# Kernel tuning notes

Measured on AMD Instinct MI355X. Metric: run time of the kernel, lower is better.

Reference implementation:

```python
import jax, jax.numpy as jnp
import numpy as np

BN_EPS = 1e-5


def setup_inputs() -> dict:
    key = jax.random.key(0)
    ks = jax.random.split(key, 8)
    B, N, D = 16, 16384, 64
    NP, NS = 1024, 32
    inp = {
        "xyz": jax.random.normal(ks[0], (B, 3, N), dtype=jnp.float32),
        "points": jax.random.normal(ks[1], (B, D, N), dtype=jnp.float32),
        "fps_init": jax.random.randint(ks[2], (B,), 0, N, dtype=jnp.int32),
        "group_idx": jax.random.randint(ks[3], (B, NP, NS), 0, N, dtype=jnp.int32),
    }
    chans = [67, 64, 128, 128]
    for i in range(3):
        cin, cout = chans[i], chans[i + 1]
        wk = jax.random.fold_in(ks[4], i)
        inp[f"W{i}"] = jax.random.normal(wk, (cout, cin), dtype=jnp.float32) * (1.0 / np.sqrt(cin))
        inp[f"b{i}"] = jnp.zeros((cout,), dtype=jnp.float32)
        inp[f"g{i}"] = jnp.ones((cout,), dtype=jnp.float32)
        inp[f"be{i}"] = jnp.zeros((cout,), dtype=jnp.float32)
    return inp


def _fps(x, init_far, npoint):
    # x: [B,N,3]; iterative furthest point sampling, npoint sequential steps
    B, N, _ = x.shape

    def step(carry, _):
        dist, far = carry
        c = jnp.take_along_axis(x, far[:, None, None], axis=1)  # [B,1,3]
        d = jnp.sum((x - c) ** 2, axis=-1)                       # [B,N]
        dist = jnp.minimum(dist, d)
        return (dist, jnp.argmax(dist, axis=-1).astype(far.dtype)), far

    init = (jnp.full((B, N), 1e10, dtype=x.dtype), init_far)
    _, cents = jax.lax.scan(step, init, None, length=npoint)
    return cents.T  # [B, npoint]


def _conv_bn_relu(h, W, b, g, be):
    # h: [B, np, ns, Cin]; 1x1 conv == channel matmul; BN (training stats) over (B,np,ns)
    y = jnp.einsum('bskc,oc->bsko', h, W) + b
    m = y.mean(axis=(0, 1, 2))
    v = y.var(axis=(0, 1, 2))
    y = (y - m) * jax.lax.rsqrt(v + BN_EPS) * g + be
    return jax.nn.relu(y)


def reference(xyz, points, fps_init, group_idx,
              W0, b0, g0, be0, W1, b1, g1, be1, W2, b2, g2, be2):
    x = jnp.transpose(xyz, (0, 2, 1))     # [B,N,3]
    p = jnp.transpose(points, (0, 2, 1))  # [B,N,D]
    B, N, _ = x.shape
    NP, NS = group_idx.shape[1], group_idx.shape[2]

    cents = _fps(x, fps_init, NP)                                   # [B,NP]
    new_xyz = jnp.take_along_axis(x, cents[:, :, None], axis=1)     # [B,NP,3]

    flat = group_idx.reshape(B, NP * NS)
    gx = jnp.take_along_axis(x, flat[:, :, None], axis=1).reshape(B, NP, NS, 3)
    gp = jnp.take_along_axis(p, flat[:, :, None], axis=1).reshape(B, NP, NS, -1)
    h = jnp.concatenate([gx, gp], axis=-1)  # [B,NP,NS,67]

    h = _conv_bn_relu(h, W0, b0, g0, be0)
    h = _conv_bn_relu(h, W1, b1, g1, be1)
    h = _conv_bn_relu(h, W2, b2, g2, be2)
    new_points = h.max(axis=2)              # max over nsample -> [B,NP,Cout]

    return jnp.transpose(new_xyz, (0, 2, 1)), jnp.transpose(new_points, (0, 2, 1))
```

## Files before the change

kernel.cpp:

```cpp
#include <hip/hip_runtime.h>

typedef short bf16x8 __attribute__((ext_vector_type(8)));
typedef float f32x4 __attribute__((ext_vector_type(4)));
typedef float f32x2 __attribute__((ext_vector_type(2)));
typedef unsigned short u16;
typedef unsigned int u32;
typedef unsigned long long u64;

#define NPTS 16384
#define NPOINT 1024
#define STOT 524288

__device__ __forceinline__ u16 f2bf(float f){
  u32 u = __builtin_bit_cast(u32, f);
  u += 0x7fffu + ((u >> 16) & 1u);
  return (u16)(u >> 16);
}
__device__ __forceinline__ float bf2f(u16 u){
  u32 x = ((u32)u) << 16;
  return __builtin_bit_cast(float, x);
}

template<int CTRL>
__device__ __forceinline__ u64 dpp_max(u64 key){
  u32 lo = (u32)key, hi = (u32)(key >> 32);
  u32 lo1 = (u32)__builtin_amdgcn_update_dpp(0, (int)lo, CTRL, 0xf, 0xf, true);
  u32 hi1 = (u32)__builtin_amdgcn_update_dpp(0, (int)hi, CTRL, 0xf, 0xf, true);
  u64 k1 = ((u64)hi1 << 32) | (u64)lo1;
  return (k1 > key) ? k1 : key;
}

__global__ __launch_bounds__(1024) void fps_kernel(const float* __restrict__ xyz,
                                                   const int* __restrict__ finit,
                                                   float4* __restrict__ xpk_all,
                                                   float* __restrict__ out0){
  __shared__ u64 warr[2][16];
  const int b = blockIdx.x, t = threadIdx.x;
  const int wave = t >> 6, lane = t & 63;
  const float* xb = xyz + (size_t)b * 3 * NPTS;
  float4* xpk = xpk_all + (size_t)b * NPTS;
  f32x2 px[8], py[8], pz[8], dist[8];
#pragma unroll
  for (int j = 0; j < 8; j++){
    f32x2 x, y, z;
#pragma unroll
    for (int h = 0; h < 2; h++){
      int n = ((2*j + h) << 10) + t;
      x[h] = xb[n];
      y[h] = xb[NPTS + n];
      z[h] = xb[2*NPTS + n];
      xpk[n] = make_float4(x[h], y[h], z[h], 0.f);
    }
    px[j] = x; py[j] = y; pz[j] = z;
    f32x2 big = {1e10f, 1e10f};
    dist[j] = big;
  }
  if (t < 32) ((u64*)warr)[t] = 0ULL;
  const int far0 = finit[b];
  __syncthreads();
  int nbu = far0;
  for (int it = 0; it < NPOINT; it++){
    float4 cc = xpk[nbu];
    if (t == 0){
      out0[((size_t)b*3 + 0)*NPOINT + it] = cc.x;
      out0[((size_t)b*3 + 1)*NPOINT + it] = cc.y;
      out0[((size_t)b*3 + 2)*NPOINT + it] = cc.z;
    }
    float bv = -1.f; int bk = 0;
    {
#pragma clang fp contract(off)
      f32x2 cx2 = {cc.x, cc.x}, cy2 = {cc.y, cc.y}, cz2 = {cc.z, cc.z};
#pragma unroll
      for (int j = 0; j < 8; j++){
        f32x2 dx = px[j] - cx2;
        f32x2 dy = py[j] - cy2;
        f32x2 dz = pz[j] - cz2;
        f32x2 dd = dx*dx + dy*dy + dz*dz;
        f32x2 dm = __builtin_elementwise_min(dist[j], dd);
        dist[j] = dm;
        bool g0 = dm.x > bv;
        bv = g0 ? dm.x : bv;  bk = g0 ? (2*j)   : bk;
        bool g1 = dm.y > bv;
        bv = g1 ? dm.y : bv;  bk = g1 ? (2*j+1) : bk;
      }
    }
    int bi = (bk << 10) + t;
    u64 key = ((u64)__builtin_bit_cast(u32, bv) << 32) | (u64)(u32)(~(u32)bi);
    key = dpp_max<0xB1>(key);
    key = dpp_max<0x4E>(key);
    key = dpp_max<0x141>(key);
    key = dpp_max<0x140>(key);
    key = dpp_max<0x142>(key);
    key = dpp_max<0x143>(key);
    if (lane == 63) warr[it & 1][wave] = key;
    __syncthreads();
    u64 kv = warr[it & 1][lane & 15];
    kv = dpp_max<0xB1>(kv);
    kv = dpp_max<0x4E>(kv);
    kv = dpp_max<0x141>(kv);
    kv = dpp_max<0x140>(kv);
    int nb = (int)(~(u32)kv);
    nbu = __builtin_amdgcn_readfirstlane(nb);
  }
}

__global__ __launch_bounds__(256) void pack_kernel(const float* __restrict__ xyz,
                                                   const float* __restrict__ points,
                                                   u16* __restrict__ XP){
  __shared__ float ldsb[67*256];
  const int blk = blockIdx.x, t = threadIdx.x;
  const int b = blk >> 6;
  const int n0 = (blk & 63) << 8;
  for (int c = 0; c < 67; c++){
    const float* src = (c < 3) ? (xyz + ((size_t)b*3 + c)*NPTS)
                               : (points + ((size_t)b*64 + (c-3))*NPTS);
    ldsb[c*256 + t] = src[n0 + t];
  }
  __syncthreads();
  u16* dst = XP + ((size_t)b*NPTS + n0)*96;
  for (int itc = 0; itc < 12; itc++){
    int q = t + (itc << 8);
    int r = q / 12, ch = q % 12;
    u16 tmp[8];
#pragma unroll
    for (int j = 0; j < 8; j++){
      int c = ch*8 + j;
      tmp[j] = (c < 67) ? f2bf(ldsb[c*256 + r]) : (u16)0;
    }
    uint4 v;
    v.x = (u32)tmp[0] | ((u32)tmp[1] << 16);
    v.y = (u32)tmp[2] | ((u32)tmp[3] << 16);
    v.z = (u32)tmp[4] | ((u32)tmp[5] << 16);
    v.w = (u32)tmp[6] | ((u32)tmp[7] << 16);
    *(uint4*)(dst + q*8) = v;
  }
}

__global__ __launch_bounds__(256) void prep_small(const float* __restrict__ W0,
                                                  const float* __restrict__ W1,
                                                  const float* __restrict__ W2,
                                                  u16* __restrict__ W0bf,
                                                  u16* __restrict__ W1bf,
                                                  u16* __restrict__ W2bf,
                                                  float* __restrict__ statsF){
  const int blk = blockIdx.x, t = threadIdx.x;
  if (blk < 48){
#pragma unroll
    for (int k = 0; k < 4; k++) statsF[blk*1024 + k*256 + t] = 0.f;
  } else if (blk == 48){
    for (int i = t; i < 64*96; i += 256){
      int n = i / 96, k = i % 96;
      W0bf[i] = (k < 67) ? f2bf(W0[n*67 + k]) : (u16)0;
    }
  } else if (blk <= 50){
    for (int i = (blk-49)*256 + t; i < 128*64; i += 512) W1bf[i] = f2bf(W1[i]);
  } else if (blk <= 54){
    for (int i = (blk-51)*256 + t; i < 128*128; i += 1024) W2bf[i] = f2bf(W2[i]);
  }
}

__global__ __launch_bounds__(256) void l0_kernel(const u16* __restrict__ XP,
                                                 const int* __restrict__ gidx,
                                                 const u16* __restrict__ W0bf,
                                                 u16* __restrict__ y0,
                                                 float* __restrict__ bsum, float* __restrict__ bsqr){
  __shared__ float lsum[64], lsqr[64];
  const int blk = blockIdx.x, t = threadIdx.x;
  const int b = blk >> 8, j = blk & 255;
  const int wave = t >> 6, lane = t & 63, lrow = lane & 15, lq = lane >> 4;
  if (t < 64){ lsum[t] = 0.f; lsqr[t] = 0.f; }
  __syncthreads();
  const size_t srow = (size_t)blk * 128;
  const int m0 = wave*32 + lrow, m1 = m0 + 16;
  const int gbase = b*32768 + j*128;
  const int p0 = gidx[gbase + m0];
  const int p1 = gidx[gbase + m1];
  const bf16x8* ar0 = (const bf16x8*)(XP + ((size_t)b*NPTS + p0)*96);
  const bf16x8* ar1 = (const bf16x8*)(XP + ((size_t)b*NPTS + p1)*96);
  f32x4 acc[2][4];
#pragma unroll
  for (int mt = 0; mt < 2; mt++)
#pragma unroll
    for (int nt = 0; nt < 4; nt++){ f32x4 z = {0.f,0.f,0.f,0.f}; acc[mt][nt] = z; }
#pragma unroll
  for (int ks = 0; ks < 3; ks++){
    bf16x8 af0 = ar0[ks*4 + lq];
    bf16x8 af1 = ar1[ks*4 + lq];
#pragma unroll
    for (int nt = 0; nt < 4; nt++){
      bf16x8 bb = *(const bf16x8*)(W0bf + (nt*16 + lrow)*96 + ks*32 + lq*8);
      acc[0][nt] = __builtin_amdgcn_mfma_f32_16x16x32_bf16(af0, bb, acc[0][nt], 0, 0, 0);
      acc[1][nt] = __builtin_amdgcn_mfma_f32_16x16x32_bf16(af1, bb, acc[1][nt], 0, 0, 0);
    }
  }
#pragma unroll
  for (int nt = 0; nt < 4; nt++){
    float s = 0.f, s2 = 0.f;
#pragma unroll
    for (int mt = 0; mt < 2; mt++){
#pragma unroll
      for (int i = 0; i < 4; i++){
        float u = acc[mt][nt][i];
        s += u; s2 = fmaf(u, u, s2);
        int m = wave*32 + mt*16 + lq*4 + i;
        y0[(srow + m)*64 + nt*16 + lrow] = f2bf(u);
      }
    }
    s  += __shfl_xor(s, 16, 64);  s  += __shfl_xor(s, 32, 64);
    s2 += __shfl_xor(s2, 16, 64); s2 += __shfl_xor(s2, 32, 64);
    if (lane < 16){ atomicAdd(&lsum[nt*16 + lane], s); atomicAdd(&lsqr[nt*16 + lane], s2); }
  }
  __syncthreads();
  if (t < 64){
    int bkt = blk & 63;
    atomicAdd(&bsum[bkt*128 + t], lsum[t]);
    atomicAdd(&bsqr[bkt*128 + t], lsqr[t]);
  }
}

__global__ __launch_bounds__(128) void stats_kernel(const float* __restrict__ bsum,
                                                    const float* __restrict__ bsqr,
                                                    const float* __restrict__ g,
                                                    const float* __restrict__ be,
                                                    float* __restrict__ a, float* __restrict__ d, int C){
  const int c = threadIdx.x;
  if (c >= C) return;
  float s = 0.f, s2 = 0.f;
  for (int k = 0; k < 64; k++){ s += bsum[k*128 + c]; s2 += bsqr[k*128 + c]; }
  const float inv = 1.f / (float)STOT;
  float m = s * inv;
  float v = s2 * inv - m*m;
  float aa = g[c] / sqrtf(v + 1e-5f);
  a[c] = aa;
  d[c] = be[c] - m*aa;
}

__device__ __forceinline__ bf16x8 load_bn_relu(const u16* __restrict__ row, int ko,
                                               const float* __restrict__ av,
                                               const float* __restrict__ dv){
  uint4 r = *(const uint4*)(row + ko);
  u32 w[4] = {r.x, r.y, r.z, r.w};
  bf16x8 out;
#pragma unroll
  for (int jj = 0; jj < 8; jj++){
    u16 us = (u16)(w[jj >> 1] >> ((jj & 1) * 16));
    float h = fmaxf(fmaf(av[ko + jj], bf2f(us), dv[ko + jj]), 0.f);
    out[jj] = (short)f2bf(h);
  }
  return out;
}

__global__ __launch_bounds__(256) void l1_kernel(const u16* __restrict__ y0,
                                                 const u16* __restrict__ W1bf,
                                                 const float* __restrict__ a0, const float* __restrict__ d0,
                                                 u16* __restrict__ y1,
                                                 float* __restrict__ bsum, float* __restrict__ bsqr){
  __shared__ float lsum[128], lsqr[128];
  __shared__ float av[64], dv[64];
  const int blk = blockIdx.x, t = threadIdx.x;
  const int wave = t >> 6, lane = t & 63, lrow = lane & 15, lq = lane >> 4;
  if (t < 128){ lsum[t] = 0.f; lsqr[t] = 0.f; }
  if (t < 64){ av[t] = a0[t]; dv[t] = d0[t]; }
  __syncthreads();
  const size_t srow = (size_t)blk * 128;
  const int m0 = wave*32 + lrow, m1 = m0 + 16;
  const u16* row0 = y0 + (srow + m0)*64;
  const u16* row1 = y0 + (srow + m1)*64;
  f32x4 acc[2][8];
#pragma unroll
  for (int mt = 0; mt < 2; mt++)
#pragma unroll
    for (int nt = 0; nt < 8; nt++){ f32x4 z = {0.f,0.f,0.f,0.f}; acc[mt][nt] = z; }
#pragma unroll
  for (int ks = 0; ks < 2; ks++){
    const int ko = ks*32 + lq*8;
    bf16x8 af0 = load_bn_relu(row0, ko, av, dv);
    bf16x8 af1 = load_bn_relu(row1, ko, av, dv);
#pragma unroll
    for (int nt = 0; nt < 8; nt++){
      bf16x8 bb = *(const bf16x8*)(W1bf + (nt*16 + lrow)*64 + ko);
      acc[0][nt] = __builtin_amdgcn_mfma_f32_16x16x32_bf16(af0, bb, acc[0][nt], 0, 0, 0);
      acc[1][nt] = __builtin_amdgcn_mfma_f32_16x16x32_bf16(af1, bb, acc[1][nt], 0, 0, 0);
    }
  }
#pragma unroll
  for (int nt = 0; nt < 8; nt++){
    float s = 0.f, s2 = 0.f;
#pragma unroll
    for (int mt = 0; mt < 2; mt++){
#pragma unroll
      for (int i = 0; i < 4; i++){
        float u = acc[mt][nt][i];
        s += u; s2 = fmaf(u, u, s2);
        int m = wave*32 + mt*16 + lq*4 + i;
        y1[(srow + m)*128 + nt*16 + lrow] = f2bf(u);
      }
    }
    s  += __shfl_xor(s, 16, 64);  s  += __shfl_xor(s, 32, 64);
    s2 += __shfl_xor(s2, 16, 64); s2 += __shfl_xor(s2, 32, 64);
    if (lane < 16){ atomicAdd(&lsum[nt*16 + lane], s); atomicAdd(&lsqr[nt*16 + lane], s2); }
  }
  __syncthreads();
  if (t < 128){
    int bkt = blk & 63;
    atomicAdd(&bsum[bkt*128 + t], lsum[t]);
    atomicAdd(&bsqr[bkt*128 + t], lsqr[t]);
  }
}

__global__ __launch_bounds__(256) void l2_kernel(const u16* __restrict__ y1,
                                                 const u16* __restrict__ W2bf,
                                                 const float* __restrict__ a1, const float* __restrict__ d1,
                                                 float* __restrict__ maxb, float* __restrict__ minb,
                                                 float* __restrict__ bsum, float* __restrict__ bsqr){
  __shared__ float lsum[128], lsqr[128];
  __shared__ float av[128], dv[128];
  const int blk = blockIdx.x, t = threadIdx.x;
  const int wave = t >> 6, lane = t & 63, lrow = lane & 15, lq = lane >> 4;
  if (t < 128){ lsum[t] = 0.f; lsqr[t] = 0.f; av[t] = a1[t]; dv[t] = d1[t]; }
  __syncthreads();
  const size_t srow = (size_t)blk * 128;
  const int m0 = wave*32 + lrow, m1 = m0 + 16;
  const u16* row0 = y1 + (srow + m0)*128;
  const u16* row1 = y1 + (srow + m1)*128;
  f32x4 acc[2][8];
#pragma unroll
  for (int mt = 0; mt < 2; mt++)
#pragma unroll
    for (int nt = 0; nt < 8; nt++){ f32x4 z = {0.f,0.f,0.f,0.f}; acc[mt][nt] = z; }
#pragma unroll
  for (int ks = 0; ks < 4; ks++){
    const int ko = ks*32 + lq*8;
    bf16x8 af0 = load_bn_relu(row0, ko, av, dv);
    bf16x8 af1 = load_bn_relu(row1, ko, av, dv);
#pragma unroll
    for (int nt = 0; nt < 8; nt++){
      bf16x8 bb = *(const bf16x8*)(W2bf + (nt*16 + lrow)*128 + ko);
      acc[0][nt] = __builtin_amdgcn_mfma_f32_16x16x32_bf16(af0, bb, acc[0][nt], 0, 0, 0);
      acc[1][nt] = __builtin_amdgcn_mfma_f32_16x16x32_bf16(af1, bb, acc[1][nt], 0, 0, 0);
    }
  }
#pragma unroll
  for (int nt = 0; nt < 8; nt++){
    float s = 0.f, s2 = 0.f, mx = -3.4e38f, mn = 3.4e38f;
#pragma unroll
    for (int mt = 0; mt < 2; mt++){
#pragma unroll
      for (int i = 0; i < 4; i++){
        float u = acc[mt][nt][i];
        s += u; s2 = fmaf(u, u, s2);
        mx = fmaxf(mx, u); mn = fminf(mn, u);
      }
    }
    s  += __shfl_xor(s, 16, 64);  s  += __shfl_xor(s, 32, 64);
    s2 += __shfl_xor(s2, 16, 64); s2 += __shfl_xor(s2, 32, 64);
    mx = fmaxf(mx, __shfl_xor(mx, 16, 64)); mx = fmaxf(mx, __shfl_xor(mx, 32, 64));
    mn = fminf(mn, __shfl_xor(mn, 16, 64)); mn = fminf(mn, __shfl_xor(mn, 32, 64));
    if (lane < 16){
      size_t gi = ((size_t)blk*4 + wave)*128 + nt*16 + lane;
      maxb[gi] = mx; minb[gi] = mn;
      atomicAdd(&lsum[nt*16 + lane], s); atomicAdd(&lsqr[nt*16 + lane], s2);
    }
  }
  __syncthreads();
  if (t < 128){
    int bkt = blk & 63;
    atomicAdd(&bsum[bkt*128 + t], lsum[t]);
    atomicAdd(&bsqr[bkt*128 + t], lsqr[t]);
  }
}

__global__ __launch_bounds__(256) void final_kernel(const float* __restrict__ maxb,
                                                    const float* __restrict__ minb,
                                                    const float* __restrict__ a2, const float* __restrict__ d2,
                                                    float* __restrict__ out1){
  __shared__ float ldsb[64*129];
  __shared__ float av[128], dv[128];
  const int blk = blockIdx.x, t = threadIdx.x;
  const int b = blk >> 4, np0 = (blk & 15) << 6;
  if (t < 128){ av[t] = a2[t]; dv[t] = d2[t]; }
  __syncthreads();
  const size_t base = ((size_t)b*NPOINT + np0)*128;
  for (int itc = 0; itc < 32; itc++){
    int e = t + (itc << 8);
    int npl = e >> 7, c = e & 127;
    float a = av[c];
    float mxv = maxb[base + e], mnv = minb[base + e];
    float vsel = (a >= 0.f) ? mxv : mnv;
    ldsb[npl*129 + c] = fmaxf(fmaf(a, vsel, dv[c]), 0.f);
  }
  __syncthreads();
  for (int itc = 0; itc < 32; itc++){
    int e = t + (itc << 8);
    int c = e >> 6, npl = e & 63;
    out1[((size_t)b*128 + c)*NPOINT + np0 + npl] = ldsb[npl*129 + c];
  }
}

extern "C" void kernel_launch(void* const* d_in, const int* in_sizes, int n_in,
                              void* d_out, int out_size, void* d_ws, size_t ws_size,
                              hipStream_t stream) {
  const float* xyz    = (const float*)d_in[0];
  const float* points = (const float*)d_in[1];
  const int*   finit  = (const int*)d_in[2];
  const int*   gidx   = (const int*)d_in[3];
  const float* W0  = (const float*)d_in[4];
  const float* g0v = (const float*)d_in[6];
  const float* be0 = (const float*)d_in[7];
  const float* W1  = (const float*)d_in[8];
  const float* g1v = (const float*)d_in[10];
  const float* be1 = (const float*)d_in[11];
  const float* W2  = (const float*)d_in[12];
  const float* g2v = (const float*)d_in[14];
  const float* be2 = (const float*)d_in[15];

  float* out0 = (float*)d_out;
  float* out1 = out0 + 16*3*NPOINT;

  char* ws = (char*)d_ws;
  u16* XP = (u16*)ws;
  u16* y1 = (u16*)ws;
  u16* y0 = (u16*)(ws + 134217728);
  float4* xpk = (float4*)(ws + 134217728);
  float* maxb = (float*)(ws + 134217728);
  float* minb = (float*)(ws + 134217728 + 8388608);
  float* statsF = (float*)(ws + 201326592);
  float* bsum0 = statsF;          float* bsqr0 = statsF + 8192;
  float* bsum1 = statsF + 16384;  float* bsqr1 = statsF + 24576;
  float* bsum2 = statsF + 32768;  float* bsqr2 = statsF + 40960;
  float* a0 = statsF + 49152;       float* d0 = a0 + 128;
  float* a1 = statsF + 49152 + 256; float* d1 = a1 + 128;
  float* a2 = statsF + 49152 + 512; float* d2 = a2 + 128;
  u16* W0bf = (u16*)(statsF + 49920);
  u16* W1bf = W0bf + 64*96;
  u16* W2bf = W1bf + 128*64;

  fps_kernel<<<16, 1024, 0, stream>>>(xyz, finit, xpk, out0);
  prep_small<<<64, 256, 0, stream>>>(W0, W1, W2, W0bf, W1bf, W2bf, statsF);
  pack_kernel<<<1024, 256, 0, stream>>>(xyz, points, XP);
  l0_kernel<<<4096, 256, 0, stream>>>(XP, gidx, W0bf, y0, bsum0, bsqr0);
  stats_kernel<<<1, 128, 0, stream>>>(bsum0, bsqr0, g0v, be0, a0, d0, 64);
  l1_kernel<<<4096, 256, 0, stream>>>(y0, W1bf, a0, d0, y1, bsum1, bsqr1);
  stats_kernel<<<1, 128, 0, stream>>>(bsum1, bsqr1, g1v, be1, a1, d1, 128);
  l2_kernel<<<4096, 256, 0, stream>>>(y1, W2bf, a1, d1, maxb, minb, bsum2, bsqr2);
  stats_kernel<<<1, 128, 0, stream>>>(bsum2, bsqr2, g2v, be2, a2, d2, 128);
  final_kernel<<<256, 256, 0, stream>>>(maxb, minb, a2, d2, out1);
}
```

Measured before the change: 2.231 ms.

## Spatially sort FPS points into Morton buckets and skip far clusters

The FPS kernel now bins points into a 16^3 Morton grid, counting-sorts them so each wave owns spatially coherent clusters of 256 points, and computes a bounding sphere per cluster. Each iteration skips a cluster's distance update when the new centroid is provably too far to lower any distance below the cluster's current max, which cuts the per-iteration distance arithmetic. It adds a setup pass with LDS atomics and a prefix scan, more cross-wave partial keys, and relies on conservative bound margins to keep argmax results exact.

```diff
diff --git a/kernel.cpp b/kernel.cpp
--- a/kernel.cpp
+++ b/kernel.cpp
@@ -29,36 +29,127 @@
   u64 k1 = ((u64)hi1 << 32) | (u64)lo1;
   return (k1 > key) ? k1 : key;
 }
+__device__ __forceinline__ u64 umax64(u64 a, u64 b){ return (a > b) ? a : b; }
+__device__ __forceinline__ u64 packkey(float d, int idx){
+  return ((u64)__builtin_bit_cast(u32, d) << 32) | (u64)(u32)(~(u32)idx);
+}
+__device__ __forceinline__ u32 spread3(int v){
+  u32 x = (u32)v;
+  return (x & 1u) | ((x & 2u) << 2) | ((x & 4u) << 4) | ((x & 8u) << 6);
+}
+__device__ __forceinline__ float wred_sum(float v){
+#pragma unroll
+  for (int off = 1; off < 64; off <<= 1) v += __shfl_xor(v, off, 64);
+  return v;
+}
+__device__ __forceinline__ float wred_max(float v){
+#pragma unroll
+  for (int off = 1; off < 64; off <<= 1) v = fmaxf(v, __shfl_xor(v, off, 64));
+  return v;
+}
 
 __global__ __launch_bounds__(1024) void fps_kernel(const float* __restrict__ xyz,
                                                    const int* __restrict__ finit,
                                                    float4* __restrict__ xpk_all,
+                                                   float4* __restrict__ xps_all,
                                                    float* __restrict__ out0){
-  __shared__ u64 warr[2][16];
+  __shared__ u32 hist[4096];
+  __shared__ u32 wsum[16];
+  __shared__ u64 par[2][64];
   const int b = blockIdx.x, t = threadIdx.x;
   const int wave = t >> 6, lane = t & 63;
   const float* xb = xyz + (size_t)b * 3 * NPTS;
   float4* xpk = xpk_all + (size_t)b * NPTS;
+  float4* xps = xps_all + (size_t)b * NPTS;
+
+  for (int i = t; i < 4096; i += 1024) hist[i] = 0;
+  __syncthreads();
+  u32 cr[16];
+#pragma unroll
+  for (int k = 0; k < 16; k++){
+    int n = (k << 10) + t;
+    float x = xb[n], y = xb[NPTS + n], z = xb[2*NPTS + n];
+    xpk[n] = make_float4(x, y, z, 0.f);
+    int xi = (int)fminf(fmaxf((x + 4.5f)*1.7777778f, 0.f), 15.f);
+    int yi = (int)fminf(fmaxf((y + 4.5f)*1.7777778f, 0.f), 15.f);
+    int zi = (int)fminf(fmaxf((z + 4.5f)*1.7777778f, 0.f), 15.f);
+    u32 cell = spread3(xi) | (spread3(yi) << 1) | (spread3(zi) << 2);
+    u32 rank = atomicAdd(&hist[cell], 1u);
+    cr[k] = (cell << 16) | rank;
+  }
+  __syncthreads();
+  uint4 hv = *(const uint4*)&hist[4*t];
+  u32 s = hv.x + hv.y + hv.z + hv.w;
+  u32 sInc = s;
+#pragma unroll
+  for (int off = 1; off < 64; off <<= 1){
+    u32 nv = (u32)__shfl_up((int)sInc, off, 64);
+    if (lane >= off) sInc += nv;
+  }
+  if (lane == 63) wsum[wave] = sInc;
+  __syncthreads();
+  u32 wb = 0;
+#pragma unroll
+  for (int i = 0; i < 16; i++) if (i < wave) wb += wsum[i];
+  u32 ex = wb + sInc - s;
+  hist[4*t]   = ex;
+  hist[4*t+1] = ex + hv.x;
+  hist[4*t+2] = ex + hv.x + hv.y;
+  hist[4*t+3] = ex + hv.x + hv.y + hv.z;
+  __syncthreads();
+#pragma unroll
+  for (int k = 0; k < 16; k++){
+    int n = (k << 10) + t;
+    float4 pnt = xpk[n];
+    u32 cell = cr[k] >> 16, rank = cr[k] & 0xFFFFu;
+    u32 pos = hist[cell] + rank;
+    pnt.w = __int_as_float(n);
+    xps[pos] = pnt;
+  }
+  __syncthreads();
   f32x2 px[8], py[8], pz[8], dist[8];
-#pragma unroll
-  for (int j = 0; j < 8; j++){
-    f32x2 x, y, z;
-#pragma unroll
-    for (int h = 0; h < 2; h++){
-      int n = ((2*j + h) << 10) + t;
-      x[h] = xb[n];
-      y[h] = xb[NPTS + n];
-      z[h] = xb[2*NPTS + n];
-      xpk[n] = make_float4(x[h], y[h], z[h], 0.f);
-    }
-    px[j] = x; py[j] = y; pz[j] = z;
-    f32x2 big = {1e10f, 1e10f};
-    dist[j] = big;
-  }
-  if (t < 32) ((u64*)warr)[t] = 0ULL;
-  const int far0 = finit[b];
-  __syncthreads();
-  int nbu = far0;
+  int idxv[16];
+#pragma unroll
+  for (int q = 0; q < 4; q++){
+#pragma unroll
+    for (int jj = 0; jj < 4; jj++){
+      int pos = (wave << 10) + (q << 8) + (jj << 6) + lane;
+      float4 sp = xps[pos];
+      int pr = 2*q + (jj >> 1), hf = jj & 1;
+      px[pr][hf] = sp.x; py[pr][hf] = sp.y; pz[pr][hf] = sp.z;
+      dist[pr][hf] = 1e10f;
+      idxv[4*q + jj] = __float_as_int(sp.w);
+    }
+  }
+  float ctrx[4], ctry[4], ctrz[4], rad[4], bmax[4];
+  u64 kb[4];
+#pragma unroll
+  for (int q = 0; q < 4; q++){
+    f32x2 sx2 = px[2*q] + px[2*q+1];
+    f32x2 sy2 = py[2*q] + py[2*q+1];
+    f32x2 sz2 = pz[2*q] + pz[2*q+1];
+    float cx = wred_sum(sx2.x + sx2.y) * (1.f/256.f);
+    float cy = wred_sum(sy2.x + sy2.y) * (1.f/256.f);
+    float cz = wred_sum(sz2.x + sz2.y) * (1.f/256.f);
+    float m2 = 0.f;
+#pragma unroll
+    for (int pr = 0; pr < 2; pr++){
+#pragma unroll
+      for (int hf = 0; hf < 2; hf++){
+        float dx = px[2*q+pr][hf] - cx, dy = py[2*q+pr][hf] - cy, dz = pz[2*q+pr][hf] - cz;
+        m2 = fmaxf(m2, dx*dx + dy*dy + dz*dz);
+      }
+    }
+    m2 = wred_max(m2);
+    ctrx[q] = __builtin_bit_cast(float, __builtin_amdgcn_readfirstlane(__builtin_bit_cast(int, cx)));
+    ctry[q] = __builtin_bit_cast(float, __builtin_amdgcn_readfirstlane(__builtin_bit_cast(int, cy)));
+    ctrz[q] = __builtin_bit_cast(float, __builtin_amdgcn_readfirstlane(__builtin_bit_cast(int, cz)));
+    rad[q]  = sqrtf(m2) * 1.0001f + 1e-6f;
+    bmax[q] = 1e10f;
+    kb[q]   = 0ULL;
+  }
+  int nbu = finit[b];
+  int p = 0;
   for (int it = 0; it < NPOINT; it++){
     float4 cc = xpk[nbu];
     if (t == 0){
@@ -66,41 +157,55 @@
       out0[((size_t)b*3 + 1)*NPOINT + it] = cc.y;
       out0[((size_t)b*3 + 2)*NPOINT + it] = cc.z;
     }
-    float bv = -1.f; int bk = 0;
-    {
+#pragma unroll
+    for (int q = 0; q < 4; q++){
+      float exx = cc.x - ctrx[q], eyy = cc.y - ctry[q], ezz = cc.z - ctrz[q];
+      float sd = sqrtf(exx*exx + eyy*eyy + ezz*ezz);
+      float tt = sd * 0.999f - rad[q];
+      bool doit = !((tt > 0.f) && (tt*tt >= bmax[q]));
+      if (__builtin_amdgcn_readfirstlane((int)doit)){
+        {
 #pragma clang fp contract(off)
-      f32x2 cx2 = {cc.x, cc.x}, cy2 = {cc.y, cc.y}, cz2 = {cc.z, cc.z};
-#pragma unroll
-      for (int j = 0; j < 8; j++){
-        f32x2 dx = px[j] - cx2;
-        f32x2 dy = py[j] - cy2;
-        f32x2 dz = pz[j] - cz2;
-        f32x2 dd = dx*dx + dy*dy + dz*dz;
-        f32x2 dm = __builtin_elementwise_min(dist[j], dd);
-        dist[j] = dm;
-        bool g0 = dm.x > bv;
-        bv = g0 ? dm.x : bv;  bk = g0 ? (2*j)   : bk;
-        bool g1 = dm.y > bv;
-        bv = g1 ? dm.y : bv;  bk = g1 ? (2*j+1) : bk;
+          f32x2 cx2 = {cc.x, cc.x}, cy2 = {cc.y, cc.y}, cz2 = {cc.z, cc.z};
+#pragma unroll
+          for (int pr = 0; pr < 2; pr++){
+            int ii = 2*q + pr;
+            f32x2 dx = px[ii] - cx2;
+            f32x2 dy = py[ii] - cy2;
+            f32x2 dz = pz[ii] - cz2;
+            f32x2 dd = dx*dx + dy*dy + dz*dz;
+            dist[ii] = __builtin_elementwise_min(dist[ii], dd);
+          }
+        }
+        u64 k0 = packkey(dist[2*q].x,   idxv[4*q+0]);
+        u64 k1 = packkey(dist[2*q].y,   idxv[4*q+1]);
+        u64 k2 = packkey(dist[2*q+1].x, idxv[4*q+2]);
+        u64 k3 = packkey(dist[2*q+1].y, idxv[4*q+3]);
+        u64 km = umax64(umax64(k0, k1), umax64(k2, k3));
+        km = dpp_max<0xB1>(km);
+        km = dpp_max<0x4E>(km);
+        km = dpp_max<0x141>(km);
+        km = dpp_max<0x140>(km);
+        km = dpp_max<0x142>(km);
+        km = dpp_max<0x143>(km);
+        u32 klo = (u32)__builtin_amdgcn_readlane((int)(u32)km, 63);
+        u32 khi = (u32)__builtin_amdgcn_readlane((int)(u32)(km >> 32), 63);
+        bmax[q] = __builtin_bit_cast(float, khi) * 1.0001f;
+        kb[q] = ((u64)khi << 32) | (u64)klo;
       }
     }
-    int bi = (bk << 10) + t;
-    u64 key = ((u64)__builtin_bit_cast(u32, bv) << 32) | (u64)(u32)(~(u32)bi);
-    key = dpp_max<0xB1>(key);
-    key = dpp_max<0x4E>(key);
-    key = dpp_max<0x141>(key);
-    key = dpp_max<0x140>(key);
-    key = dpp_max<0x142>(key);
-    key = dpp_max<0x143>(key);
-    if (lane == 63) warr[it & 1][wave] = key;
+    u64 kv = (lane == 0) ? kb[0] : (lane == 1) ? kb[1] : (lane == 2) ? kb[2] : kb[3];
+    if (lane < 4) par[p][4*wave + lane] = kv;
     __syncthreads();
-    u64 kv = warr[it & 1][lane & 15];
-    kv = dpp_max<0xB1>(kv);
-    kv = dpp_max<0x4E>(kv);
-    kv = dpp_max<0x141>(kv);
-    kv = dpp_max<0x140>(kv);
-    int nb = (int)(~(u32)kv);
-    nbu = __builtin_amdgcn_readfirstlane(nb);
+    int sl = lane & 15;
+    u64 m0 = par[p][sl], m1 = par[p][sl+16], m2 = par[p][sl+32], m3 = par[p][sl+48];
+    u64 mm = umax64(umax64(m0, m1), umax64(m2, m3));
+    mm = dpp_max<0xB1>(mm);
+    mm = dpp_max<0x4E>(mm);
+    mm = dpp_max<0x141>(mm);
+    mm = dpp_max<0x140>(mm);
+    nbu = __builtin_amdgcn_readfirstlane((int)~(u32)mm);
+    p ^= 1;
   }
 }
 
@@ -422,6 +527,7 @@
   u16* y1 = (u16*)ws;
   u16* y0 = (u16*)(ws + 134217728);
   float4* xpk = (float4*)(ws + 134217728);
+  float4* xps = (float4*)(ws + 138412032);
   float* maxb = (float*)(ws + 134217728);
   float* minb = (float*)(ws + 134217728 + 8388608);
   float* statsF = (float*)(ws + 201326592);
@@ -435,7 +541,7 @@
   u16* W1bf = W0bf + 64*96;
   u16* W2bf = W1bf + 128*64;
 
-  fps_kernel<<<16, 1024, 0, stream>>>(xyz, finit, xpk, out0);
+  fps_kernel<<<16, 1024, 0, stream>>>(xyz, finit, xpk, xps, out0);
   prep_small<<<64, 256, 0, stream>>>(W0, W1, W2, W0bf, W1bf, W2bf, statsF);
   pack_kernel<<<1024, 256, 0, stream>>>(xyz, points, XP);
   l0_kernel<<<4096, 256, 0, stream>>>(XP, gidx, W0bf, y0, bsum0, bsqr0);
```

New measurement: 2.703 ms. 21.1% more time.
